# Kernel tuning notes

Measured on AMD Instinct MI355X. Metric: run time of the kernel, lower is better.

Reference implementation:

```python
import jax, jax.numpy as jnp
import numpy as np

HID = 101
IN = 3


def lstm_cell(x, h, c, W_ih, W_hh, b_ih, b_hh):
    # PyTorch LSTMCell gate order: i, f, g, o
    gates = x @ W_ih.T + b_ih + h @ W_hh.T + b_hh  # [B, 4H]
    i, f, g, o = jnp.split(gates, 4, axis=-1)
    i = jax.nn.sigmoid(i)
    f = jax.nn.sigmoid(f)
    g = jnp.tanh(g)
    o = jax.nn.sigmoid(o)
    c_new = f * c + i * g
    h_new = o * jnp.tanh(c_new)
    return h_new, c_new


def setup_inputs() -> dict:
    key = jax.random.key(0)
    ks = jax.random.split(key, 12)
    B, T = 1024, 256
    s1 = 1.0 / np.sqrt(HID)
    u = lambda k, shp: jax.random.uniform(k, shp, jnp.float32, -s1, s1)
    return {
        "input": jax.random.normal(ks[0], (B, T, IN), jnp.float32),
        "W_ih1": u(ks[1], (4 * HID, IN)),
        "W_hh1": u(ks[2], (4 * HID, HID)),
        "b_ih1": u(ks[3], (4 * HID,)),
        "b_hh1": u(ks[4], (4 * HID,)),
        "W_ih2": u(ks[5], (4 * HID, HID)),
        "W_hh2": u(ks[6], (4 * HID, HID)),
        "b_ih2": u(ks[7], (4 * HID,)),
        "b_hh2": u(ks[8], (4 * HID,)),
        "Wl": u(ks[9], (IN, HID)),
        "bl": u(ks[10], (IN,)),
        "future": 32,
    }


def reference(input, W_ih1, W_hh1, b_ih1, b_hh1, W_ih2, W_hh2, b_ih2, b_hh2, Wl, bl, future):
    B = input.shape[0]
    h1 = jnp.zeros((B, HID), input.dtype)
    c1 = jnp.zeros((B, HID), input.dtype)
    h2 = jnp.zeros((B, HID), input.dtype)
    c2 = jnp.zeros((B, HID), input.dtype)

    def step(carry, x_t):
        h1, c1, h2, c2 = carry
        h1, c1 = lstm_cell(x_t, h1, c1, W_ih1, W_hh1, b_ih1, b_hh1)
        h2, c2 = lstm_cell(h1, h2, c2, W_ih2, W_hh2, b_ih2, b_hh2)
        out = h2 @ Wl.T + bl  # [B, 3]
        return (h1, c1, h2, c2), out

    xs = jnp.transpose(input, (1, 0, 2))  # [T, B, 3]
    carry, outs = jax.lax.scan(step, (h1, c1, h2, c2), xs)

    if future > 0:
        last_out = outs[-1]

        def fstep(carry, _):
            h1, c1, h2, c2, out = carry
            h1, c1 = lstm_cell(out, h1, c1, W_ih1, W_hh1, b_ih1, b_hh1)
            h2, c2 = lstm_cell(h1, h2, c2, W_ih2, W_hh2, b_ih2, b_hh2)
            out = h2 @ Wl.T + bl
            return (h1, c1, h2, c2, out), out

        _, fouts = jax.lax.scan(fstep, (*carry, last_out), None, length=future)
        outs = jnp.concatenate([outs, fouts], axis=0)

    return jnp.transpose(outs, (1, 0, 2))  # [B, T+future, 3]
```

## Files before the change

kernel.cpp:

```cpp
#include <hip/hip_runtime.h>
#include <hip/hip_bf16.h>

#define HID 101
#define BATCH 1024
#define RPB 4
#define NBLK 256
#define NTHR 512
#define TSEQ 256

#define A1SZ  (7*4*4*512)
#define A2SZ  (7*4*7*512)
#define A2OFF A1SZ
#define AOOFF (A1SZ + A2SZ)
#define AOSZ  (4*512)

typedef _Float16 h8 __attribute__((ext_vector_type(8)));
typedef float f4 __attribute__((ext_vector_type(4)));

__global__ void prep_kernel(const float* __restrict__ W_ih1, const float* __restrict__ W_hh1,
                            const float* __restrict__ b_ih1, const float* __restrict__ b_hh1,
                            const float* __restrict__ W_ih2, const float* __restrict__ W_hh2,
                            const float* __restrict__ b_ih2, const float* __restrict__ b_hh2,
                            const float* __restrict__ Wl, _Float16* __restrict__ wsA) {
    int idx = blockIdx.x * blockDim.x + threadIdx.x;
    int stride = gridDim.x * blockDim.x;
    for (int t = idx; t < A1SZ; t += stride) {
        int i = t & 7, lane = (t >> 3) & 63, kt = (t >> 9) & 3, tau = (t >> 11) & 3, w = t >> 13;
        int k = kt * 32 + ((lane >> 4) & 3) * 8 + i;
        int u = 16 * w + (lane & 15);
        float v = 0.f;
        if (u < HID) {
            int g = tau * HID + u;
            if (k < HID) v = W_hh1[g * HID + k];
            else if (k >= 101 && k <= 103) v = W_ih1[g * 3 + (k - 101)];
            else if (k == 104) v = b_ih1[g] + b_hh1[g];
        }
        wsA[t] = (_Float16)v;
    }
    for (int t = idx; t < A2SZ; t += stride) {
        int i = t & 7, lane = (t >> 3) & 63;
        int rem = t >> 9;
        int kt = rem % 7; rem /= 7;
        int tau = rem & 3, w = rem >> 2;
        int k = kt * 32 + ((lane >> 4) & 3) * 8 + i;
        int u = 16 * w + (lane & 15);
        float v = 0.f;
        if (u < HID) {
            int g = tau * HID + u;
            if (k < HID) v = W_ih2[g * HID + k];
            else if (k == 104) v = b_ih2[g] + b_hh2[g];
            else if (k >= 112 && k < 213) v = W_hh2[g * HID + (k - 112)];
        }
        wsA[A2OFF + t] = (_Float16)v;
    }
    for (int t = idx; t < AOSZ; t += stride) {
        int i = t & 7, lane = (t >> 3) & 63, kk = (t >> 9) & 3;
        int k = (kk + 3) * 32 + ((lane >> 4) & 3) * 8 + i;
        int j = lane & 15;
        float v = (j < 3 && k >= 112 && k < 213) ? Wl[j * HID + (k - 112)] : 0.f;
        wsA[AOOFF + t] = (_Float16)v;
    }
}

__device__ __forceinline__ float sigm(float z) {
    return __builtin_amdgcn_rcpf(1.f + __expf(-z));
}
__device__ __forceinline__ float tanhf_(float z) {
    return 1.f - 2.f * __builtin_amdgcn_rcpf(__expf(2.f * z) + 1.f);
}

#define MFMA(acc, a, b) acc = __builtin_amdgcn_mfma_f32_16x16x32_f16(a, b, acc, 0, 0, 0)

__global__ __launch_bounds__(NTHR, 2) void lstm_kernel(
    const float* __restrict__ input, const _Float16* __restrict__ wsA,
    const float* __restrict__ bl, int steps, float* __restrict__ out)
{
    const int tid = threadIdx.x;
    const int wid = tid >> 6, lane = tid & 63;
    const int q = lane >> 4, col = lane & 15;
    const int r0 = blockIdx.x * RPB;
    const int ostride = steps * 3;

    __shared__ _Float16 Sb[2][3584];
    __shared__ float zwA[7][4][4][16];
    __shared__ float zwB[7][4][4][16];
    __shared__ _Float16 xpre[TSEQ * 12];

    h8 A1[4][4];
    h8 A2[4][7];
    if (wid < 7) {
        #pragma unroll
        for (int tau = 0; tau < 4; tau++) {
            #pragma unroll
            for (int kt = 0; kt < 4; kt++)
                A1[tau][kt] = *(const volatile h8*)(
                    wsA + ((size_t)((wid * 4 + tau) * 4 + kt) * 512 + lane * 8));
            #pragma unroll
            for (int kt = 0; kt < 7; kt++)
                A2[tau][kt] = *(const volatile h8*)(
                    wsA + (size_t)A2OFF + ((size_t)((wid * 4 + tau) * 7 + kt) * 512 + lane * 8));
        }
    } else {
        #pragma unroll
        for (int kt = 0; kt < 4; kt++)
            A2[0][kt] = *(const volatile h8*)(
                wsA + (size_t)AOOFF + ((size_t)(kt) * 512 + lane * 8));
    }
    const float bl0 = bl[0], bl1 = bl[1], bl2 = bl[2];

    const int r_ew = lane & 3, ul = lane >> 2;
    const int u = 16 * wid + ul;
    const bool ewv = (wid < 7) && (u < HID);
    const int hs1 = (u >> 3) * 128 + r_ew * 8 + (u & 7);
    const int hs2 = (14 + (u >> 3)) * 128 + r_ew * 8 + (u & 7);
    const int boff = q * 128 + col * 8;
    const int xr = lane / 3, xj = lane - 3 * xr;
    const int xoff = 12 * 128 + xr * 8 + 5 + xj;

    for (int i2 = tid; i2 < 3584; i2 += NTHR) {
        Sb[0][i2] = (_Float16)0.f; Sb[1][i2] = (_Float16)0.f;
    }
    for (int g = tid; g < RPB * TSEQ * 3; g += NTHR) {
        int r = g / (TSEQ * 3), rem = g - r * (TSEQ * 3);
        int tt = rem / 3, j = rem - 3 * tt;
        xpre[tt * 12 + r * 3 + j] = (_Float16)input[(size_t)(r0 + r) * (TSEQ * 3) + rem];
    }
    __syncthreads();
    if (tid < 16) {
        Sb[0][13 * 128 + tid * 8] = (_Float16)1.0f;
        Sb[1][13 * 128 + tid * 8] = (_Float16)1.0f;
    }
    if (tid < 12) {
        int r = tid / 3, j = tid - 3 * (tid / 3);
        Sb[0][12 * 128 + r * 8 + 5 + j] = xpre[r * 3 + j];
    }
    float c1 = 0.f, c2 = 0.f;
    __syncthreads();

    for (int t = 0; t < TSEQ; ++t) {
        _Float16* Rb = Sb[t & 1];
        _Float16* Wt = Sb[1 - (t & 1)];
        if (wid < 7) {
            h8 bf0 = (_Float16)0.f, bf1 = bf0, bf2 = bf0, bf3 = bf0,
               bf4 = bf0, bf5 = bf0, bf6 = bf0;
            if (col < 4) {
                bf0 = *(const h8*)(Rb + 0 * 512 + boff);
                bf1 = *(const h8*)(Rb + 1 * 512 + boff);
                bf2 = *(const h8*)(Rb + 2 * 512 + boff);
                bf3 = *(const h8*)(Rb + 3 * 512 + boff);
                bf4 = *(const h8*)(Rb + 4 * 512 + boff);
                bf5 = *(const h8*)(Rb + 5 * 512 + boff);
                bf6 = *(const h8*)(Rb + 6 * 512 + boff);
            }
            f4 a0 = {0.f,0.f,0.f,0.f}, a1 = a0, a2 = a0, a3 = a0;
            MFMA(a0, A1[0][0], bf0); MFMA(a1, A1[1][0], bf0); MFMA(a2, A1[2][0], bf0); MFMA(a3, A1[3][0], bf0);
            MFMA(a0, A1[0][1], bf1); MFMA(a1, A1[1][1], bf1); MFMA(a2, A1[2][1], bf1); MFMA(a3, A1[3][1], bf1);
            MFMA(a0, A1[0][2], bf2); MFMA(a1, A1[1][2], bf2); MFMA(a2, A1[2][2], bf2); MFMA(a3, A1[3][2], bf2);
            MFMA(a0, A1[0][3], bf3); MFMA(a1, A1[1][3], bf3); MFMA(a2, A1[2][3], bf3); MFMA(a3, A1[3][3], bf3);
            if (col < 4) {
                *(f4*)&zwA[wid][0][col][4 * q] = a0;
                *(f4*)&zwA[wid][1][col][4 * q] = a1;
                *(f4*)&zwA[wid][2][col][4 * q] = a2;
                *(f4*)&zwA[wid][3][col][4 * q] = a3;
            }
            if (t >= 1) {
                f4 b0 = {0.f,0.f,0.f,0.f}, b1 = b0, b2 = b0, b3 = b0;
                MFMA(b0, A2[0][0], bf0); MFMA(b1, A2[1][0], bf0); MFMA(b2, A2[2][0], bf0); MFMA(b3, A2[3][0], bf0);
                MFMA(b0, A2[0][1], bf1); MFMA(b1, A2[1][1], bf1); MFMA(b2, A2[2][1], bf1); MFMA(b3, A2[3][1], bf1);
                MFMA(b0, A2[0][2], bf2); MFMA(b1, A2[1][2], bf2); MFMA(b2, A2[2][2], bf2); MFMA(b3, A2[3][2], bf2);
                MFMA(b0, A2[0][3], bf3); MFMA(b1, A2[1][3], bf3); MFMA(b2, A2[2][3], bf3); MFMA(b3, A2[3][3], bf3);
                MFMA(b0, A2[0][4], bf4); MFMA(b1, A2[1][4], bf4); MFMA(b2, A2[2][4], bf4); MFMA(b3, A2[3][4], bf4);
                MFMA(b0, A2[0][5], bf5); MFMA(b1, A2[1][5], bf5); MFMA(b2, A2[2][5], bf5); MFMA(b3, A2[3][5], bf5);
                MFMA(b0, A2[0][6], bf6); MFMA(b1, A2[1][6], bf6); MFMA(b2, A2[2][6], bf6); MFMA(b3, A2[3][6], bf6);
                if (col < 4) {
                    *(f4*)&zwB[wid][0][col][4 * q] = b0;
                    *(f4*)&zwB[wid][1][col][4 * q] = b1;
                    *(f4*)&zwB[wid][2][col][4 * q] = b2;
                    *(f4*)&zwB[wid][3][col][4 * q] = b3;
                }
            }
            {
                float z0 = zwA[wid][0][r_ew][ul], z1 = zwA[wid][1][r_ew][ul];
                float z2 = zwA[wid][2][r_ew][ul], z3 = zwA[wid][3][r_ew][ul];
                float ig = sigm(z0), fg = sigm(z1), gg = tanhf_(z2), og = sigm(z3);
                c1 = fg * c1 + ig * gg;
                float h1v = og * tanhf_(c1);
                if (ewv) Wt[hs1] = (_Float16)h1v;
            }
            if (t >= 1) {
                float z0 = zwB[wid][0][r_ew][ul], z1 = zwB[wid][1][r_ew][ul];
                float z2 = zwB[wid][2][r_ew][ul], z3 = zwB[wid][3][r_ew][ul];
                float ig = sigm(z0), fg = sigm(z1), gg = tanhf_(z2), og = sigm(z3);
                c2 = fg * c2 + ig * gg;
                float h2v = og * tanhf_(c2);
                if (ewv) Wt[hs2] = (_Float16)h2v;
            }
        } else {
            if (t >= 2) {
                f4 ao = {0.f, 0.f, 0.f, 0.f};
                #pragma unroll
                for (int kk = 0; kk < 4; kk++) {
                    h8 b = (_Float16)0.f;
                    if (col < 4) b = *(const h8*)(Rb + (kk + 3) * 512 + boff);
                    MFMA(ao, A2[0][kk], b);
                }
                if (lane < 4) {
                    float* op = out + (size_t)(r0 + lane) * ostride + (size_t)(t - 2) * 3;
                    op[0] = ao[0] + bl0; op[1] = ao[1] + bl1; op[2] = ao[2] + bl2;
                }
            }
            if (t + 1 < TSEQ && lane < 12)
                Wt[xoff] = xpre[(t + 1) * 12 + xr * 3 + xj];
        }
        __syncthreads();
    }

    {
        _Float16* Rb = Sb[0];
        _Float16* Wt = Sb[1];
        if (wid < 7) {
            h8 bf0 = (_Float16)0.f, bf1 = bf0, bf2 = bf0, bf3 = bf0,
               bf4 = bf0, bf5 = bf0, bf6 = bf0;
            if (col < 4) {
                bf0 = *(const h8*)(Rb + 0 * 512 + boff);
                bf1 = *(const h8*)(Rb + 1 * 512 + boff);
                bf2 = *(const h8*)(Rb + 2 * 512 + boff);
                bf3 = *(const h8*)(Rb + 3 * 512 + boff);
                bf4 = *(const h8*)(Rb + 4 * 512 + boff);
                bf5 = *(const h8*)(Rb + 5 * 512 + boff);
                bf6 = *(const h8*)(Rb + 6 * 512 + boff);
            }
            f4 b0 = {0.f,0.f,0.f,0.f}, b1 = b0, b2 = b0, b3 = b0;
            MFMA(b0, A2[0][0], bf0); MFMA(b1, A2[1][0], bf0); MFMA(b2, A2[2][0], bf0); MFMA(b3, A2[3][0], bf0);
            MFMA(b0, A2[0][1], bf1); MFMA(b1, A2[1][1], bf1); MFMA(b2, A2[2][1], bf1); MFMA(b3, A2[3][1], bf1);
            MFMA(b0, A2[0][2], bf2); MFMA(b1, A2[1][2], bf2); MFMA(b2, A2[2][2], bf2); MFMA(b3, A2[3][2], bf2);
            MFMA(b0, A2[0][3], bf3); MFMA(b1, A2[1][3], bf3); MFMA(b2, A2[2][3], bf3); MFMA(b3, A2[3][3], bf3);
            MFMA(b0, A2[0][4], bf4); MFMA(b1, A2[1][4], bf4); MFMA(b2, A2[2][4], bf4); MFMA(b3, A2[3][4], bf4);
            MFMA(b0, A2[0][5], bf5); MFMA(b1, A2[1][5], bf5); MFMA(b2, A2[2][5], bf5); MFMA(b3, A2[3][5], bf5);
            MFMA(b0, A2[0][6], bf6); MFMA(b1, A2[1][6], bf6); MFMA(b2, A2[2][6], bf6); MFMA(b3, A2[3][6], bf6);
            if (col < 4) {
                *(f4*)&zwB[wid][0][col][4 * q] = b0;
                *(f4*)&zwB[wid][1][col][4 * q] = b1;
                *(f4*)&zwB[wid][2][col][4 * q] = b2;
                *(f4*)&zwB[wid][3][col][4 * q] = b3;
            }
            float z0 = zwB[wid][0][r_ew][ul], z1 = zwB[wid][1][r_ew][ul];
            float z2 = zwB[wid][2][r_ew][ul], z3 = zwB[wid][3][r_ew][ul];
            float ig = sigm(z0), fg = sigm(z1), gg = tanhf_(z2), og = sigm(z3);
            c2 = fg * c2 + ig * gg;
            float h2v = og * tanhf_(c2);
            if (ewv) Wt[hs2] = (_Float16)h2v;
        } else {
            f4 ao = {0.f, 0.f, 0.f, 0.f};
            #pragma unroll
            for (int kk = 0; kk < 4; kk++) {
                h8 b = (_Float16)0.f;
                if (col < 4) b = *(const h8*)(Rb + (kk + 3) * 512 + boff);
                MFMA(ao, A2[0][kk], b);
            }
            if (lane < 4) {
                float* op = out + (size_t)(r0 + lane) * ostride + (size_t)(TSEQ - 2) * 3;
                op[0] = ao[0] + bl0; op[1] = ao[1] + bl1; op[2] = ao[2] + bl2;
            }
        }
        __syncthreads();
    }

    for (int t = TSEQ; t < steps; ++t) {
        _Float16* R = Sb[t & 1];
        _Float16* W = Sb[1 - (t & 1)];
        if (wid == 7) {
            f4 ao = {0.f, 0.f, 0.f, 0.f};
            #pragma unroll
            for (int kk = 0; kk < 4; kk++) {
                h8 b = (_Float16)0.f;
                if (col < 4) b = *(const h8*)(W + (kk + 3) * 512 + boff);
                MFMA(ao, A2[0][kk], b);
            }
            if (lane < 4) {
                float o0 = ao[0] + bl0, o1 = ao[1] + bl1, o2 = ao[2] + bl2;
                float* op = out + (size_t)(r0 + lane) * ostride + (size_t)(t - 1) * 3;
                op[0] = o0; op[1] = o1; op[2] = o2;
                R[12 * 128 + lane * 8 + 5] = (_Float16)o0;
                R[12 * 128 + lane * 8 + 6] = (_Float16)o1;
                R[12 * 128 + lane * 8 + 7] = (_Float16)o2;
            }
        }
        __syncthreads();
        if (wid < 7) {
            f4 a0 = {0.f,0.f,0.f,0.f}, a1 = a0, a2 = a0, a3 = a0;
            #pragma unroll
            for (int kt = 0; kt < 4; kt++) {
                h8 b = (_Float16)0.f;
                if (col < 4) b = *(const h8*)(R + kt * 512 + boff);
                MFMA(a0, A1[0][kt], b); MFMA(a1, A1[1][kt], b);
                MFMA(a2, A1[2][kt], b); MFMA(a3, A1[3][kt], b);
            }
            if (col < 4) {
                *(f4*)&zwA[wid][0][col][4 * q] = a0;
                *(f4*)&zwA[wid][1][col][4 * q] = a1;
                *(f4*)&zwA[wid][2][col][4 * q] = a2;
                *(f4*)&zwA[wid][3][col][4 * q] = a3;
            }
            float z0 = zwA[wid][0][r_ew][ul], z1 = zwA[wid][1][r_ew][ul];
            float z2 = zwA[wid][2][r_ew][ul], z3 = zwA[wid][3][r_ew][ul];
            float ig = sigm(z0), fg = sigm(z1), gg = tanhf_(z2), og = sigm(z3);
            c1 = fg * c1 + ig * gg;
            float h1v = og * tanhf_(c1);
            if (ewv) W[hs1] = (_Float16)h1v;
        }
        __syncthreads();
        if (wid < 7) {
            f4 b0 = {0.f,0.f,0.f,0.f}, b1 = b0, b2 = b0, b3 = b0;
            #pragma unroll
            for (int kt = 0; kt < 7; kt++) {
                h8 b = (_Float16)0.f;
                if (col < 4) b = *(const h8*)(W + kt * 512 + boff);
                MFMA(b0, A2[0][kt], b); MFMA(b1, A2[1][kt], b);
                MFMA(b2, A2[2][kt], b); MFMA(b3, A2[3][kt], b);
            }
            if (col < 4) {
                *(f4*)&zwB[wid][0][col][4 * q] = b0;
                *(f4*)&zwB[wid][1][col][4 * q] = b1;
                *(f4*)&zwB[wid][2][col][4 * q] = b2;
                *(f4*)&zwB[wid][3][col][4 * q] = b3;
            }
            float z0 = zwB[wid][0][r_ew][ul], z1 = zwB[wid][1][r_ew][ul];
            float z2 = zwB[wid][2][r_ew][ul], z3 = zwB[wid][3][r_ew][ul];
            float ig = sigm(z0), fg = sigm(z1), gg = tanhf_(z2), og = sigm(z3);
            c2 = fg * c2 + ig * gg;
            float h2v = og * tanhf_(c2);
            if (ewv) R[hs2] = (_Float16)h2v;
        }
        __syncthreads();
    }

    if (wid == 7) {
        f4 ao = {0.f, 0.f, 0.f, 0.f};
        #pragma unroll
        for (int kk = 0; kk < 4; kk++) {
            h8 b = (_Float16)0.f;
            if (col < 4) b = *(const h8*)(&Sb[1][0] + (kk + 3) * 512 + boff);
            MFMA(ao, A2[0][kk], b);
        }
        if (lane < 4) {
            float* op = out + (size_t)(r0 + lane) * ostride + (size_t)(steps - 1) * 3;
            op[0] = ao[0] + bl0; op[1] = ao[1] + bl1; op[2] = ao[2] + bl2;
        }
    }
}

extern "C" void kernel_launch(void* const* d_in, const int* in_sizes, int n_in,
                              void* d_out, int out_size, void* d_ws, size_t ws_size,
                              hipStream_t stream) {
    const float* input = (const float*)d_in[0];
    const float* W_ih1 = (const float*)d_in[1];
    const float* W_hh1 = (const float*)d_in[2];
    const float* b_ih1 = (const float*)d_in[3];
    const float* b_hh1 = (const float*)d_in[4];
    const float* W_ih2 = (const float*)d_in[5];
    const float* W_hh2 = (const float*)d_in[6];
    const float* b_ih2 = (const float*)d_in[7];
    const float* b_hh2 = (const float*)d_in[8];
    const float* Wl    = (const float*)d_in[9];
    const float* bl    = (const float*)d_in[10];
    int steps = out_size / (BATCH * 3);
    _Float16* wsA = (_Float16*)d_ws;

    hipLaunchKernelGGL(prep_kernel, dim3(512), dim3(256), 0, stream,
                       W_ih1, W_hh1, b_ih1, b_hh1, W_ih2, W_hh2, b_ih2, b_hh2, Wl, wsA);
    hipLaunchKernelGGL(lstm_kernel, dim3(NBLK), dim3(NTHR), 0, stream,
                       input, wsA, bl, steps, (float*)d_out);
}
```

Measured before the change: 398.0 us.

## Apply LSTM gates directly on MFMA accumulators, dropping LDS gate round-trip

Removes the zwA/zwB shared-memory staging of gate pre-activations. Each lane now applies the gate nonlinearities to the four accumulator elements it already holds from the MFMA output and writes packed fp16 h values. To allow those vector writes, the shared h/x buffer layout changes to a padded 160-element quad stride, and the bias and input slot offsets are remapped to match. This saves LDS stores and loads plus the bank traffic on the serial recurrence path. In exchange each lane computes four elements instead of one, including for idle columns, and the new layout must exactly match the prepacked weight ordering.

```diff
diff --git a/kernel.cpp b/kernel.cpp
--- a/kernel.cpp
+++ b/kernel.cpp
@@ -15,6 +15,7 @@
 #define AOSZ  (4*512)
 
 typedef _Float16 h8 __attribute__((ext_vector_type(8)));
+typedef _Float16 h4 __attribute__((ext_vector_type(4)));
 typedef float f4 __attribute__((ext_vector_type(4)));
 
 __global__ void prep_kernel(const float* __restrict__ W_ih1, const float* __restrict__ W_hh1,
@@ -71,6 +72,10 @@
 
 #define MFMA(acc, a, b) acc = __builtin_amdgcn_mfma_f32_16x16x32_f16(a, b, acc, 0, 0, 0)
 
+__device__ __forceinline__ int SLOT(int k, int col) {
+    return (k >> 5) * 512 + ((k >> 3) & 3) * 160 + col * 8 + (k & 7);
+}
+
 __global__ __launch_bounds__(NTHR, 2) void lstm_kernel(
     const float* __restrict__ input, const _Float16* __restrict__ wsA,
     const float* __restrict__ bl, int steps, float* __restrict__ out)
@@ -82,8 +87,6 @@
     const int ostride = steps * 3;
 
     __shared__ _Float16 Sb[2][3584];
-    __shared__ float zwA[7][4][4][16];
-    __shared__ float zwB[7][4][4][16];
     __shared__ _Float16 xpre[TSEQ * 12];
 
     h8 A1[4][4];
@@ -108,14 +111,13 @@
     }
     const float bl0 = bl[0], bl1 = bl[1], bl2 = bl[2];
 
-    const int r_ew = lane & 3, ul = lane >> 2;
-    const int u = 16 * wid + ul;
-    const bool ewv = (wid < 7) && (u < HID);
-    const int hs1 = (u >> 3) * 128 + r_ew * 8 + (u & 7);
-    const int hs2 = (14 + (u >> 3)) * 128 + r_ew * 8 + (u & 7);
-    const int boff = q * 128 + col * 8;
+    const int boff = q * 160 + col * 8;
+    const int uu0 = 16 * wid + 4 * q;
+    const int nv = HID - uu0;
+    const int slot1 = SLOT(uu0, col);
+    const int slot2 = SLOT(112 + uu0, col);
     const int xr = lane / 3, xj = lane - 3 * xr;
-    const int xoff = 12 * 128 + xr * 8 + 5 + xj;
+    const int xoff = 1536 + xr * 8 + 5 + xj;
 
     for (int i2 = tid; i2 < 3584; i2 += NTHR) {
         Sb[0][i2] = (_Float16)0.f; Sb[1][i2] = (_Float16)0.f;
@@ -126,16 +128,35 @@
         xpre[tt * 12 + r * 3 + j] = (_Float16)input[(size_t)(r0 + r) * (TSEQ * 3) + rem];
     }
     __syncthreads();
-    if (tid < 16) {
-        Sb[0][13 * 128 + tid * 8] = (_Float16)1.0f;
-        Sb[1][13 * 128 + tid * 8] = (_Float16)1.0f;
+    if (tid < 4) {
+        Sb[0][1696 + tid * 8] = (_Float16)1.0f;
+        Sb[1][1696 + tid * 8] = (_Float16)1.0f;
     }
     if (tid < 12) {
         int r = tid / 3, j = tid - 3 * (tid / 3);
-        Sb[0][12 * 128 + r * 8 + 5 + j] = xpre[r * 3 + j];
-    }
-    float c1 = 0.f, c2 = 0.f;
+        Sb[0][1536 + r * 8 + 5 + j] = xpre[r * 3 + j];
+    }
+    float c1e[4] = {0.f, 0.f, 0.f, 0.f}, c2e[4] = {0.f, 0.f, 0.f, 0.f};
     __syncthreads();
+
+    auto EWST = [&](const f4& a0, const f4& a1, const f4& a2, const f4& a3,
+                    float* c, _Float16* dst, int slot) {
+        float hv[4];
+        #pragma unroll
+        for (int e = 0; e < 4; e++) {
+            float ig = sigm(a0[e]), fg = sigm(a1[e]), gg = tanhf_(a2[e]), og = sigm(a3[e]);
+            c[e] = fg * c[e] + ig * gg;
+            hv[e] = og * tanhf_(c[e]);
+        }
+        if (col < 4 && nv > 0) {
+            if (nv >= 4) {
+                h4 hp = { (_Float16)hv[0], (_Float16)hv[1], (_Float16)hv[2], (_Float16)hv[3] };
+                *(h4*)(dst + slot) = hp;
+            } else {
+                dst[slot] = (_Float16)hv[0];
+            }
+        }
+    };
 
     for (int t = 0; t < TSEQ; ++t) {
         _Float16* Rb = Sb[t & 1];
@@ -157,14 +178,8 @@
             MFMA(a0, A1[0][1], bf1); MFMA(a1, A1[1][1], bf1); MFMA(a2, A1[2][1], bf1); MFMA(a3, A1[3][1], bf1);
             MFMA(a0, A1[0][2], bf2); MFMA(a1, A1[1][2], bf2); MFMA(a2, A1[2][2], bf2); MFMA(a3, A1[3][2], bf2);
             MFMA(a0, A1[0][3], bf3); MFMA(a1, A1[1][3], bf3); MFMA(a2, A1[2][3], bf3); MFMA(a3, A1[3][3], bf3);
-            if (col < 4) {
-                *(f4*)&zwA[wid][0][col][4 * q] = a0;
-                *(f4*)&zwA[wid][1][col][4 * q] = a1;
-                *(f4*)&zwA[wid][2][col][4 * q] = a2;
-                *(f4*)&zwA[wid][3][col][4 * q] = a3;
-            }
+            f4 b0 = {0.f,0.f,0.f,0.f}, b1 = b0, b2 = b0, b3 = b0;
             if (t >= 1) {
-                f4 b0 = {0.f,0.f,0.f,0.f}, b1 = b0, b2 = b0, b3 = b0;
                 MFMA(b0, A2[0][0], bf0); MFMA(b1, A2[1][0], bf0); MFMA(b2, A2[2][0], bf0); MFMA(b3, A2[3][0], bf0);
                 MFMA(b0, A2[0][1], bf1); MFMA(b1, A2[1][1], bf1); MFMA(b2, A2[2][1], bf1); MFMA(b3, A2[3][1], bf1);
                 MFMA(b0, A2[0][2], bf2); MFMA(b1, A2[1][2], bf2); MFMA(b2, A2[2][2], bf2); MFMA(b3, A2[3][2], bf2);
@@ -172,29 +187,9 @@
                 MFMA(b0, A2[0][4], bf4); MFMA(b1, A2[1][4], bf4); MFMA(b2, A2[2][4], bf4); MFMA(b3, A2[3][4], bf4);
                 MFMA(b0, A2[0][5], bf5); MFMA(b1, A2[1][5], bf5); MFMA(b2, A2[2][5], bf5); MFMA(b3, A2[3][5], bf5);
                 MFMA(b0, A2[0][6], bf6); MFMA(b1, A2[1][6], bf6); MFMA(b2, A2[2][6], bf6); MFMA(b3, A2[3][6], bf6);
-                if (col < 4) {
-                    *(f4*)&zwB[wid][0][col][4 * q] = b0;
-                    *(f4*)&zwB[wid][1][col][4 * q] = b1;
-                    *(f4*)&zwB[wid][2][col][4 * q] = b2;
-                    *(f4*)&zwB[wid][3][col][4 * q] = b3;
-                }
-            }
-            {
-                float z0 = zwA[wid][0][r_ew][ul], z1 = zwA[wid][1][r_ew][ul];
-                float z2 = zwA[wid][2][r_ew][ul], z3 = zwA[wid][3][r_ew][ul];
-                float ig = sigm(z0), fg = sigm(z1), gg = tanhf_(z2), og = sigm(z3);
-                c1 = fg * c1 + ig * gg;
-                float h1v = og * tanhf_(c1);
-                if (ewv) Wt[hs1] = (_Float16)h1v;
-            }
-            if (t >= 1) {
-                float z0 = zwB[wid][0][r_ew][ul], z1 = zwB[wid][1][r_ew][ul];
-                float z2 = zwB[wid][2][r_ew][ul], z3 = zwB[wid][3][r_ew][ul];
-                float ig = sigm(z0), fg = sigm(z1), gg = tanhf_(z2), og = sigm(z3);
-                c2 = fg * c2 + ig * gg;
-                float h2v = og * tanhf_(c2);
-                if (ewv) Wt[hs2] = (_Float16)h2v;
-            }
+            }
+            EWST(a0, a1, a2, a3, c1e, Wt, slot1);
+            if (t >= 1) EWST(b0, b1, b2, b3, c2e, Wt, slot2);
         } else {
             if (t >= 2) {
                 f4 ao = {0.f, 0.f, 0.f, 0.f};
@@ -219,37 +214,15 @@
         _Float16* Rb = Sb[0];
         _Float16* Wt = Sb[1];
         if (wid < 7) {
-            h8 bf0 = (_Float16)0.f, bf1 = bf0, bf2 = bf0, bf3 = bf0,
-               bf4 = bf0, bf5 = bf0, bf6 = bf0;
-            if (col < 4) {
-                bf0 = *(const h8*)(Rb + 0 * 512 + boff);
-                bf1 = *(const h8*)(Rb + 1 * 512 + boff);
-                bf2 = *(const h8*)(Rb + 2 * 512 + boff);
-                bf3 = *(const h8*)(Rb + 3 * 512 + boff);
-                bf4 = *(const h8*)(Rb + 4 * 512 + boff);
-                bf5 = *(const h8*)(Rb + 5 * 512 + boff);
-                bf6 = *(const h8*)(Rb + 6 * 512 + boff);
-            }
             f4 b0 = {0.f,0.f,0.f,0.f}, b1 = b0, b2 = b0, b3 = b0;
-            MFMA(b0, A2[0][0], bf0); MFMA(b1, A2[1][0], bf0); MFMA(b2, A2[2][0], bf0); MFMA(b3, A2[3][0], bf0);
-            MFMA(b0, A2[0][1], bf1); MFMA(b1, A2[1][1], bf1); MFMA(b2, A2[2][1], bf1); MFMA(b3, A2[3][1], bf1);
-            MFMA(b0, A2[0][2], bf2); MFMA(b1, A2[1][2], bf2); MFMA(b2, A2[2][2], bf2); MFMA(b3, A2[3][2], bf2);
-            MFMA(b0, A2[0][3], bf3); MFMA(b1, A2[1][3], bf3); MFMA(b2, A2[2][3], bf3); MFMA(b3, A2[3][3], bf3);
-            MFMA(b0, A2[0][4], bf4); MFMA(b1, A2[1][4], bf4); MFMA(b2, A2[2][4], bf4); MFMA(b3, A2[3][4], bf4);
-            MFMA(b0, A2[0][5], bf5); MFMA(b1, A2[1][5], bf5); MFMA(b2, A2[2][5], bf5); MFMA(b3, A2[3][5], bf5);
-            MFMA(b0, A2[0][6], bf6); MFMA(b1, A2[1][6], bf6); MFMA(b2, A2[2][6], bf6); MFMA(b3, A2[3][6], bf6);
-            if (col < 4) {
-                *(f4*)&zwB[wid][0][col][4 * q] = b0;
-                *(f4*)&zwB[wid][1][col][4 * q] = b1;
-                *(f4*)&zwB[wid][2][col][4 * q] = b2;
-                *(f4*)&zwB[wid][3][col][4 * q] = b3;
-            }
-            float z0 = zwB[wid][0][r_ew][ul], z1 = zwB[wid][1][r_ew][ul];
-            float z2 = zwB[wid][2][r_ew][ul], z3 = zwB[wid][3][r_ew][ul];
-            float ig = sigm(z0), fg = sigm(z1), gg = tanhf_(z2), og = sigm(z3);
-            c2 = fg * c2 + ig * gg;
-            float h2v = og * tanhf_(c2);
-            if (ewv) Wt[hs2] = (_Float16)h2v;
+            #pragma unroll
+            for (int kt = 0; kt < 7; kt++) {
+                h8 b = (_Float16)0.f;
+                if (col < 4) b = *(const h8*)(Rb + kt * 512 + boff);
+                MFMA(b0, A2[0][kt], b); MFMA(b1, A2[1][kt], b);
+                MFMA(b2, A2[2][kt], b); MFMA(b3, A2[3][kt], b);
+            }
+            EWST(b0, b1, b2, b3, c2e, Wt, slot2);
         } else {
             f4 ao = {0.f, 0.f, 0.f, 0.f};
             #pragma unroll
@@ -281,9 +254,9 @@
                 float o0 = ao[0] + bl0, o1 = ao[1] + bl1, o2 = ao[2] + bl2;
                 float* op = out + (size_t)(r0 + lane) * ostride + (size_t)(t - 1) * 3;
                 op[0] = o0; op[1] = o1; op[2] = o2;
-                R[12 * 128 + lane * 8 + 5] = (_Float16)o0;
-                R[12 * 128 + lane * 8 + 6] = (_Float16)o1;
-                R[12 * 128 + lane * 8 + 7] = (_Float16)o2;
+                R[1536 + lane * 8 + 5] = (_Float16)o0;
+                R[1536 + lane * 8 + 6] = (_Float16)o1;
+                R[1536 + lane * 8 + 7] = (_Float16)o2;
             }
         }
         __syncthreads();
@@ -296,18 +269,7 @@
                 MFMA(a0, A1[0][kt], b); MFMA(a1, A1[1][kt], b);
                 MFMA(a2, A1[2][kt], b); MFMA(a3, A1[3][kt], b);
             }
-            if (col < 4) {
-                *(f4*)&zwA[wid][0][col][4 * q] = a0;
-                *(f4*)&zwA[wid][1][col][4 * q] = a1;
-                *(f4*)&zwA[wid][2][col][4 * q] = a2;
-                *(f4*)&zwA[wid][3][col][4 * q] = a3;
-            }
-            float z0 = zwA[wid][0][r_ew][ul], z1 = zwA[wid][1][r_ew][ul];
-            float z2 = zwA[wid][2][r_ew][ul], z3 = zwA[wid][3][r_ew][ul];
-            float ig = sigm(z0), fg = sigm(z1), gg = tanhf_(z2), og = sigm(z3);
-            c1 = fg * c1 + ig * gg;
-            float h1v = og * tanhf_(c1);
-            if (ewv) W[hs1] = (_Float16)h1v;
+            EWST(a0, a1, a2, a3, c1e, W, slot1);
         }
         __syncthreads();
         if (wid < 7) {
@@ -319,18 +281,7 @@
                 MFMA(b0, A2[0][kt], b); MFMA(b1, A2[1][kt], b);
                 MFMA(b2, A2[2][kt], b); MFMA(b3, A2[3][kt], b);
             }
-            if (col < 4) {
-                *(f4*)&zwB[wid][0][col][4 * q] = b0;
-                *(f4*)&zwB[wid][1][col][4 * q] = b1;
-                *(f4*)&zwB[wid][2][col][4 * q] = b2;
-                *(f4*)&zwB[wid][3][col][4 * q] = b3;
-            }
-            float z0 = zwB[wid][0][r_ew][ul], z1 = zwB[wid][1][r_ew][ul];
-            float z2 = zwB[wid][2][r_ew][ul], z3 = zwB[wid][3][r_ew][ul];
-            float ig = sigm(z0), fg = sigm(z1), gg = tanhf_(z2), og = sigm(z3);
-            c2 = fg * c2 + ig * gg;
-            float h2v = og * tanhf_(c2);
-            if (ewv) R[hs2] = (_Float16)h2v;
+            EWST(b0, b1, b2, b3, c2e, R, slot2);
         }
         __syncthreads();
     }
```

New measurement: 532.7 us. 1.34x slower.
